# Optimization experiments

Measured on AMD Instinct MI355X. Metric: run time of the kernel, lower is better.

Reference implementation:

```python
import jax, jax.numpy as jnp
import numpy as np

N_NODES = 100000
N_EDGES = 1200000
IN_FEATS = 64
OUT_FEATS = 64


def setup_inputs() -> dict:
    key = jax.random.key(0)
    k1, k2, k3, k4 = jax.random.split(key, 4)
    feature = jax.random.normal(k1, (N_NODES, IN_FEATS), dtype=jnp.float32)
    edge_src = jax.random.randint(k2, (N_EDGES,), 0, N_NODES, dtype=jnp.int32)
    edge_dst = jax.random.randint(k3, (N_EDGES,), 0, N_NODES, dtype=jnp.int32)
    # xavier_normal_ init for linear weight (fan_in=fan_out=64)
    std = float(np.sqrt(2.0 / (IN_FEATS + OUT_FEATS)))
    W = jax.random.normal(k4, (OUT_FEATS, IN_FEATS), dtype=jnp.float32) * std
    b = jnp.zeros((OUT_FEATS,), dtype=jnp.float32)
    return {"feature": feature, "edge_src": edge_src, "edge_dst": edge_dst, "W": W, "b": b}


def reference(feature, edge_src, edge_dst, W, b):
    # copy_src: gather source-node features per edge, then mean-reduce by dst.
    msgs = feature[edge_src]                                   # [E, d_in]
    summed = jax.ops.segment_sum(msgs, edge_dst, num_segments=N_NODES)  # [N, d_in]
    deg = jax.ops.segment_sum(jnp.ones((edge_src.shape[0],), feature.dtype),
                              edge_dst, num_segments=N_NODES)  # [N]
    h = summed / jnp.maximum(deg, 1.0)[:, None]                # mean; 0 for isolated nodes
    # apply_nodes: linear + activation
    h = jnp.einsum("nd,od->no", h, W) + b
    return jax.nn.relu(h)
```

## Files before the change

### kernel.cpp

```cpp
#include <hip/hip_runtime.h>


typedef __attribute__((ext_vector_type(8))) short short8;
typedef __attribute__((ext_vector_type(4))) float floatx4;

constexpr int kNodes = 100000;
constexpr int kEdges = 1200000;

constexpr int kBuckets = 1024;
constexpr int kBucketNodes = 98;

constexpr int kBinBlocks = 128;
constexpr int kEdgesPerBlock = kEdges / kBinBlocks;
constexpr int kEPT = (kEdgesPerBlock + 1023) / 1024;

constexpr int kCap = 2048;
constexpr float kFxScale = 262144.0f;
constexpr int kAccStride = 68;

constexpr int kWsFeat   = 0;
constexpr int kWsOff    = 3200000;
constexpr int kWsBinned = kWsOff + kBinBlocks * (kBuckets + 1);

__device__ __forceinline__ unsigned bf16rne(float f) {
  unsigned u = __float_as_uint(f);
  return (u + 0x7fffu + ((u >> 16) & 1u)) >> 16;
}

__global__ __launch_bounds__(1024) void gcn_build(
    const float* __restrict__ feat,
    const int* __restrict__ src, const int* __restrict__ dst,
    int* __restrict__ ws) {
  uint2* fb16  = (uint2*)(ws + kWsFeat);
  int* offT   = ws + kWsOff;
  int* binned = ws + kWsBinned;

  __shared__ int lhist[kBuckets];
  __shared__ int sm[1024];
  __shared__ int lcur[kBuckets];

  const int tid = threadIdx.x;
  lhist[tid] = 0;
  __syncthreads();

  const int e0 = blockIdx.x * kEdgesPerBlock;
  int es[kEPT], ebk[kEPT], edl[kEPT];
  #pragma unroll
  for (int k = 0; k < kEPT; ++k) {
    const int j = tid + k * 1024;
    if (j < kEdgesPerBlock) {
      es[k] = src[e0 + j];
      const int d = dst[e0 + j];
      const int bk = d / kBucketNodes;
      ebk[k] = bk;
      edl[k] = d - bk * kBucketNodes;
      atomicAdd(&lhist[bk], 1);
    }
  }

  const int t = blockIdx.x * 1024 + tid;
  for (int i = t; i < kNodes * 16; i += kBinBlocks * 1024) {
    const float* fr = feat + (size_t)(i >> 4) * 64 + (i & 15);
    uint2 p;
    p.x = bf16rne(fr[0])  | (bf16rne(fr[16]) << 16);
    p.y = bf16rne(fr[32]) | (bf16rne(fr[48]) << 16);
    fb16[i] = p;
  }
  __syncthreads();

  const int own = lhist[tid];
  sm[tid] = own;
  __syncthreads();
  for (int off = 1; off < 1024; off <<= 1) {
    int v = (tid >= off) ? sm[tid - off] : 0;
    __syncthreads();
    sm[tid] += v;
    __syncthreads();
  }
  const int excl = sm[tid] - own;
  lcur[tid] = excl;
  offT[blockIdx.x * (kBuckets + 1) + tid] = excl;
  if (tid == 0) offT[blockIdx.x * (kBuckets + 1) + kBuckets] = kEdgesPerBlock;
  __syncthreads();

  int* myBin = binned + blockIdx.x * kEdgesPerBlock;
  #pragma unroll
  for (int k = 0; k < kEPT; ++k) {
    const int j = tid + k * 1024;
    if (j < kEdgesPerBlock) {
      const int pos = atomicAdd(&lcur[ebk[k]], 1);
      myBin[pos] = es[k] | (edl[k] << 17);
    }
  }
}

__global__ __launch_bounds__(1024) void gcn_aggregate(
    const int*   __restrict__ ws_in,
    const float* __restrict__ W,
    const float* __restrict__ b,
    float*       __restrict__ out) {
  const uint2* fb16  = (const uint2*)(ws_in + kWsFeat);
  const int* offT   = ws_in + kWsOff;
  const int* binned = ws_in + kWsBinned;

  __shared__ __align__(16) char uShared[112 * 72 * 2];
  __shared__ int    accum[kBucketNodes * kAccStride];
  __shared__ int    lofs[129];
  __shared__ int    lcur[128];
  __shared__ int    runL[kBinBlocks + 1];
  __shared__ int    runG[kBinBlocks];
  __shared__ int    ssm[kBinBlocks];
  __shared__ ushort Wb16[64 * 64];
  __shared__ float  bsh[64];
  int*    lsrc  = (int*)uShared;
  ushort* hsAll = (ushort*)uShared;

  const int tid = threadIdx.x;
  const int bkt = blockIdx.x;

  if (tid < 128) lcur[tid] = 0;
  for (int i = tid; i < 4096; i += 1024) Wb16[i] = (ushort)bf16rne(W[i]);
  if (tid < 64) bsh[tid] = b[tid];
  for (int i = tid; i < kBucketNodes * kAccStride; i += 1024) accum[i] = 0;

  int len = 0;
  if (tid < kBinBlocks) {
    const int o0 = offT[tid * (kBuckets + 1) + bkt];
    const int o1 = offT[tid * (kBuckets + 1) + bkt + 1];
    len = o1 - o0;
    runG[tid] = tid * kEdgesPerBlock + o0;
    ssm[tid] = len;
  }
  __syncthreads();
  for (int off = 1; off < kBinBlocks; off <<= 1) {
    int v = 0;
    if (tid < kBinBlocks && tid >= off) v = ssm[tid - off];
    __syncthreads();
    if (tid < kBinBlocks) ssm[tid] += v;
    __syncthreads();
  }
  if (tid < kBinBlocks) runL[tid] = ssm[tid] - len;
  if (tid == kBinBlocks - 1) runL[kBinBlocks] = ssm[kBinBlocks - 1];
  __syncthreads();

  int sz = runL[kBinBlocks];
  if (sz > kCap) sz = kCap;

  auto mapRead = [&](int j) -> unsigned {
    int lo = 0, hi = kBinBlocks;
    #pragma unroll
    for (int it = 0; it < 7; ++it) {
      const int mid = (lo + hi) >> 1;
      if (runL[mid] <= j) lo = mid; else hi = mid;
    }
    return (unsigned)binned[runG[lo] + (j - runL[lo])];
  };

  const int j0 = tid, j1 = tid + 1024;
  const bool va = j0 < sz, vb = j1 < sz;
  unsigned ea = 0, eb = 0;
  if (va) { ea = mapRead(j0); atomicAdd(&lcur[ea >> 17], 1); }
  if (vb) { eb = mapRead(j1); atomicAdd(&lcur[eb >> 17], 1); }
  __syncthreads();

  if (tid < 64) {
    const int a  = lcur[tid * 2];
    const int b2 = lcur[tid * 2 + 1];
    int s = a + b2;
    #pragma unroll
    for (int off = 1; off < 64; off <<= 1) {
      const int v = __shfl_up(s, off, 64);
      if (tid >= off) s += v;
    }
    const int ex1 = s - b2;
    const int ex0 = ex1 - a;
    lofs[tid * 2]     = ex0;
    lofs[tid * 2 + 1] = ex1;
    lcur[tid * 2]     = ex0;
    lcur[tid * 2 + 1] = ex1;
    if (tid == 63) lofs[128] = s;
  }
  __syncthreads();

  if (va) { const int p = atomicAdd(&lcur[ea >> 17], 1); lsrc[p] = (int)ea; }
  if (vb) { const int p = atomicAdd(&lcur[eb >> 17], 1); lsrc[p] = (int)eb; }
  __syncthreads();

  const int wave = tid >> 6;
  const int lane = tid & 63;
  const int g = lane >> 4;
  const int c = lane & 15;
  {
    const int slot = wave * 4 + g;
    const int jb = (sz * slot) >> 6;
    const int je = (sz * (slot + 1)) >> 6;
    for (int j = jb; j < je; ++j) {
      const unsigned e = (unsigned)lsrc[j];
      const int s  = (int)(e & 0x1FFFF);
      const int dL = (int)(e >> 17);
      const uint2 v = fb16[(size_t)s * 16 + c];
      int* row = accum + dL * kAccStride + c;
      atomicAdd(row + 0,  (int)(__uint_as_float(v.x << 16)          * kFxScale));
      atomicAdd(row + 16, (int)(__uint_as_float(v.x & 0xffff0000u) * kFxScale));
      atomicAdd(row + 32, (int)(__uint_as_float(v.y << 16)          * kFxScale));
      atomicAdd(row + 48, (int)(__uint_as_float(v.y & 0xffff0000u) * kFxScale));
    }
  }
  __syncthreads();

  {
    const int nd = tid >> 3;
    const int ch = tid & 7;
    if (nd < kBucketNodes) {
      const int dg = lofs[nd + 1] - lofs[nd];
      const float inv = 1.0f / (kFxScale * (float)(dg > 1 ? dg : 1));
      const int* arow = accum + nd * kAccStride + ch * 8;
      unsigned h[8];
      #pragma unroll
      for (int q = 0; q < 8; ++q) h[q] = bf16rne((float)arow[q] * inv);
      uint4 pk;
      pk.x = h[0] | (h[1] << 16);
      pk.y = h[2] | (h[3] << 16);
      pk.z = h[4] | (h[5] << 16);
      pk.w = h[6] | (h[7] << 16);
      *(uint4*)(hsAll + nd * 72 + ch * 8) = pk;
    } else {
      if (nd < 112) *(uint4*)(hsAll + nd * 72 + ch * 8) =
          make_uint4(0u, 0u, 0u, 0u);
    }
  }
  __syncthreads();

  if (tid < 448) {
    const int w8   = tid >> 6;
    const int ln   = tid & 63;
    const int quad = ln >> 4;
    const int col  = ln & 15;
    const int n0 = bkt * kBucketNodes;

    const short8 af0 = *reinterpret_cast<const short8*>(
        hsAll + (w8 * 16 + col) * 72 + 0 * 32 + quad * 8);
    const short8 af1 = *reinterpret_cast<const short8*>(
        hsAll + (w8 * 16 + col) * 72 + 1 * 32 + quad * 8);

    #pragma unroll
    for (int ob = 0; ob < 4; ++ob) {
      const short8 bf0 = *reinterpret_cast<const short8*>(
          Wb16 + (ob * 16 + col) * 64 + 0 * 32 + quad * 8);
      const short8 bf1 = *reinterpret_cast<const short8*>(
          Wb16 + (ob * 16 + col) * 64 + 1 * 32 + quad * 8);
      floatx4 acc = {0.f, 0.f, 0.f, 0.f};
      acc = __builtin_amdgcn_mfma_f32_16x16x32_bf16(af0, bf0, acc, 0, 0, 0);
      acc = __builtin_amdgcn_mfma_f32_16x16x32_bf16(af1, bf1, acc, 0, 0, 0);

      const int o = ob * 16 + col;
      const float bo = bsh[o];
      #pragma unroll
      for (int r = 0; r < 4; ++r) {
        const int local = w8 * 16 + quad * 4 + r;
        const int node = n0 + local;
        if (local < kBucketNodes && node < kNodes) {
          const float v = acc[r] + bo;
          out[(size_t)node * 64 + o] = v > 0.0f ? v : 0.0f;
        }
      }
    }
  }
}

extern "C" void kernel_launch(void* const* d_in, const int* in_sizes, int n_in,
                              void* d_out, int out_size, void* d_ws, size_t ws_size,
                              hipStream_t stream) {
  const float* feature  = (const float*)d_in[0];
  const int*   edge_src = (const int*)  d_in[1];
  const int*   edge_dst = (const int*)  d_in[2];
  const float* W        = (const float*)d_in[3];
  const float* b        = (const float*)d_in[4];

  float* out = (float*)d_out;
  int*   ws  = (int*)d_ws;

  gcn_build<<<kBinBlocks, 1024, 0, stream>>>(feature, edge_src, edge_dst, ws);
  gcn_aggregate<<<kBuckets, 1024, 0, stream>>>(ws, W, b, out);
}
```

Baseline: 137.6 us.

## Store features as 16-bit fixed point and drop local per-node edge sort

Features are quantized in the build kernel to 16-bit signed fixed point (scale 4096) instead of bf16, so the aggregate loop can add them into the integer accumulators without float conversions. The aggregate kernel no longer counts, prefix-sums and scatters edges into a sorted shared-memory list. Each thread group now binary-searches its starting run once, walks the binned edges straight from global memory, and counts degrees with a shared atomic. This removes several barriers and shared-memory passes, at the cost of coarser precision and clamping of features beyond about ±8.

```diff
diff --git a/kernel.cpp b/kernel.cpp
--- a/kernel.cpp
+++ b/kernel.cpp
@@ -15,7 +15,7 @@
 constexpr int kEPT = (kEdgesPerBlock + 1023) / 1024;
 
 constexpr int kCap = 2048;
-constexpr float kFxScale = 262144.0f;
+constexpr float kFxScale = 4096.0f;
 constexpr int kAccStride = 68;
 
 constexpr int kWsFeat   = 0;
@@ -25,13 +25,17 @@
 __device__ __forceinline__ unsigned bf16rne(float f) {
   unsigned u = __float_as_uint(f);
   return (u + 0x7fffu + ((u >> 16) & 1u)) >> 16;
+}
+
+__device__ __forceinline__ unsigned fx16(float f) {
+  return (unsigned)(__float2int_rn(f * kFxScale)) & 0xffffu;
 }
 
 __global__ __launch_bounds__(1024) void gcn_build(
     const float* __restrict__ feat,
     const int* __restrict__ src, const int* __restrict__ dst,
     int* __restrict__ ws) {
-  uint2* fb16  = (uint2*)(ws + kWsFeat);
+  uint2* ftab = (uint2*)(ws + kWsFeat);
   int* offT   = ws + kWsOff;
   int* binned = ws + kWsBinned;
 
@@ -62,9 +66,9 @@
   for (int i = t; i < kNodes * 16; i += kBinBlocks * 1024) {
     const float* fr = feat + (size_t)(i >> 4) * 64 + (i & 15);
     uint2 p;
-    p.x = bf16rne(fr[0])  | (bf16rne(fr[16]) << 16);
-    p.y = bf16rne(fr[32]) | (bf16rne(fr[48]) << 16);
-    fb16[i] = p;
+    p.x = fx16(fr[0])  | (fx16(fr[16]) << 16);
+    p.y = fx16(fr[32]) | (fx16(fr[48]) << 16);
+    ftab[i] = p;
   }
   __syncthreads();
 
@@ -99,26 +103,23 @@
     const float* __restrict__ W,
     const float* __restrict__ b,
     float*       __restrict__ out) {
-  const uint2* fb16  = (const uint2*)(ws_in + kWsFeat);
+  const uint2* ftab  = (const uint2*)(ws_in + kWsFeat);
   const int* offT   = ws_in + kWsOff;
   const int* binned = ws_in + kWsBinned;
 
-  __shared__ __align__(16) char uShared[112 * 72 * 2];
+  __shared__ ushort hsAll[112 * 72];
   __shared__ int    accum[kBucketNodes * kAccStride];
-  __shared__ int    lofs[129];
-  __shared__ int    lcur[128];
+  __shared__ int    lcnt[128];
   __shared__ int    runL[kBinBlocks + 1];
   __shared__ int    runG[kBinBlocks];
   __shared__ int    ssm[kBinBlocks];
   __shared__ ushort Wb16[64 * 64];
   __shared__ float  bsh[64];
-  int*    lsrc  = (int*)uShared;
-  ushort* hsAll = (ushort*)uShared;
 
   const int tid = threadIdx.x;
   const int bkt = blockIdx.x;
 
-  if (tid < 128) lcur[tid] = 0;
+  if (tid < 128) lcnt[tid] = 0;
   for (int i = tid; i < 4096; i += 1024) Wb16[i] = (ushort)bf16rne(W[i]);
   if (tid < 64) bsh[tid] = b[tid];
   for (int i = tid; i < kBucketNodes * kAccStride; i += 1024) accum[i] = 0;
@@ -145,46 +146,6 @@
 
   int sz = runL[kBinBlocks];
   if (sz > kCap) sz = kCap;
-
-  auto mapRead = [&](int j) -> unsigned {
-    int lo = 0, hi = kBinBlocks;
-    #pragma unroll
-    for (int it = 0; it < 7; ++it) {
-      const int mid = (lo + hi) >> 1;
-      if (runL[mid] <= j) lo = mid; else hi = mid;
-    }
-    return (unsigned)binned[runG[lo] + (j - runL[lo])];
-  };
-
-  const int j0 = tid, j1 = tid + 1024;
-  const bool va = j0 < sz, vb = j1 < sz;
-  unsigned ea = 0, eb = 0;
-  if (va) { ea = mapRead(j0); atomicAdd(&lcur[ea >> 17], 1); }
-  if (vb) { eb = mapRead(j1); atomicAdd(&lcur[eb >> 17], 1); }
-  __syncthreads();
-
-  if (tid < 64) {
-    const int a  = lcur[tid * 2];
-    const int b2 = lcur[tid * 2 + 1];
-    int s = a + b2;
-    #pragma unroll
-    for (int off = 1; off < 64; off <<= 1) {
-      const int v = __shfl_up(s, off, 64);
-      if (tid >= off) s += v;
-    }
-    const int ex1 = s - b2;
-    const int ex0 = ex1 - a;
-    lofs[tid * 2]     = ex0;
-    lofs[tid * 2 + 1] = ex1;
-    lcur[tid * 2]     = ex0;
-    lcur[tid * 2 + 1] = ex1;
-    if (tid == 63) lofs[128] = s;
-  }
-  __syncthreads();
-
-  if (va) { const int p = atomicAdd(&lcur[ea >> 17], 1); lsrc[p] = (int)ea; }
-  if (vb) { const int p = atomicAdd(&lcur[eb >> 17], 1); lsrc[p] = (int)eb; }
-  __syncthreads();
 
   const int wave = tid >> 6;
   const int lane = tid & 63;
@@ -194,16 +155,29 @@
     const int slot = wave * 4 + g;
     const int jb = (sz * slot) >> 6;
     const int je = (sz * (slot + 1)) >> 6;
+
+    int lo = 0, hi = kBinBlocks;
+    #pragma unroll
+    for (int it = 0; it < 7; ++it) {
+      const int mid = (lo + hi) >> 1;
+      if (runL[mid] <= jb) lo = mid; else hi = mid;
+    }
+    int run  = lo;
+    int rEnd = runL[run + 1];
+    int base = runG[run] - runL[run];
+
     for (int j = jb; j < je; ++j) {
-      const unsigned e = (unsigned)lsrc[j];
+      while (j >= rEnd) { ++run; rEnd = runL[run + 1]; base = runG[run] - runL[run]; }
+      const unsigned e = (unsigned)binned[base + j];
       const int s  = (int)(e & 0x1FFFF);
       const int dL = (int)(e >> 17);
-      const uint2 v = fb16[(size_t)s * 16 + c];
+      const uint2 v = ftab[(size_t)s * 16 + c];
       int* row = accum + dL * kAccStride + c;
-      atomicAdd(row + 0,  (int)(__uint_as_float(v.x << 16)          * kFxScale));
-      atomicAdd(row + 16, (int)(__uint_as_float(v.x & 0xffff0000u) * kFxScale));
-      atomicAdd(row + 32, (int)(__uint_as_float(v.y << 16)          * kFxScale));
-      atomicAdd(row + 48, (int)(__uint_as_float(v.y & 0xffff0000u) * kFxScale));
+      atomicAdd(row + 0,  (int)(short)(v.x & 0xffffu));
+      atomicAdd(row + 16, ((int)v.x) >> 16);
+      atomicAdd(row + 32, (int)(short)(v.y & 0xffffu));
+      atomicAdd(row + 48, ((int)v.y) >> 16);
+      if (c == 0) atomicAdd(&lcnt[dL], 1);
     }
   }
   __syncthreads();
@@ -212,7 +186,7 @@
     const int nd = tid >> 3;
     const int ch = tid & 7;
     if (nd < kBucketNodes) {
-      const int dg = lofs[nd + 1] - lofs[nd];
+      const int dg = lcnt[nd];
       const float inv = 1.0f / (kFxScale * (float)(dg > 1 ? dg : 1));
       const int* arow = accum + nd * kAccStride + ch * 8;
       unsigned h[8];
@@ -224,9 +198,8 @@
       pk.z = h[4] | (h[5] << 16);
       pk.w = h[6] | (h[7] << 16);
       *(uint4*)(hsAll + nd * 72 + ch * 8) = pk;
-    } else {
-      if (nd < 112) *(uint4*)(hsAll + nd * 72 + ch * 8) =
-          make_uint4(0u, 0u, 0u, 0u);
+    } else if (nd < 112) {
+      *(uint4*)(hsAll + nd * 72 + ch * 8) = make_uint4(0u, 0u, 0u, 0u);
     }
   }
   __syncthreads();
```

After: 145.9 us. 1.06x slower.
